# Kernel tuning notes

Measured on AMD Instinct MI355X. Metric: run time of the kernel, lower is better.

Reference implementation:

```python
import jax, jax.numpy as jnp
import numpy as np

N_HEADS, EMB_DIM, K_DIM, V_DIM = 16, 1024, 64, 64
B, L = 4, 2048


def setup_inputs() -> dict:
    key = jax.random.key(0)
    ks = jax.random.split(key, 7)
    scale = 1.0 / np.sqrt(EMB_DIM)
    return {
        "query": jax.random.normal(ks[0], (B, L, EMB_DIM), dtype=jnp.float32),
        "key": jax.random.normal(ks[1], (B, L, EMB_DIM), dtype=jnp.float32),
        "value": jax.random.normal(ks[2], (B, L, EMB_DIM), dtype=jnp.float32),
        "pad_mask": jnp.ones((B, L), dtype=jnp.int32),
        # Linear weights stored as (in, out); torch Linear computes x @ W.T with W (out, in)
        "Wq": jax.random.normal(ks[3], (EMB_DIM, N_HEADS * K_DIM), dtype=jnp.float32) * scale,
        "Wk": jax.random.normal(ks[4], (EMB_DIM, N_HEADS * K_DIM), dtype=jnp.float32) * scale,
        "Wv": jax.random.normal(ks[5], (EMB_DIM, N_HEADS * V_DIM), dtype=jnp.float32) * scale,
        "Wo": jax.random.normal(ks[6], (N_HEADS * V_DIM, EMB_DIM), dtype=jnp.float32) * scale,
    }


def reference(query, key, value, pad_mask, Wq, Wk, Wv, Wo):
    batch, Lq, _ = query.shape
    Lk = key.shape[1]
    # projections -> [B, L, H, dk/dv]
    q = (query @ Wq).reshape(batch, Lq, N_HEADS, K_DIM)
    k = (key @ Wk).reshape(batch, Lk, N_HEADS, K_DIM)
    v = (value @ Wv).reshape(batch, Lk, N_HEADS, V_DIM)
    # logits: [B, H, Lq, Lk], scaled by 1/sqrt(dk)
    logits = jnp.einsum("bqhd,bkhd->bhqk", q, k) / np.sqrt(K_DIM).astype(np.float32)
    # causal mask: disallow j > i
    causal = jnp.tril(jnp.ones((Lq, Lk), dtype=bool))
    logits = jnp.where(causal[None, None], logits, -jnp.inf)
    # pad mask: positions with pad_mask == 0 are masked out
    keep = (pad_mask != 0)[:, None, None, :]  # [B,1,1,Lk]
    logits = jnp.where(keep, logits, -jnp.inf)
    probs = jax.nn.softmax(logits, axis=-1)
    attn = jnp.einsum("bhqk,bkhd->bqhd", probs, v).reshape(batch, Lq, N_HEADS * V_DIM)
    return attn @ Wo
```

## Files before the change

### kernel.cpp

```cpp
#include <hip/hip_runtime.h>
#include <hip/hip_bf16.h>

typedef short bf16x8 __attribute__((ext_vector_type(8)));
typedef float f32x4 __attribute__((ext_vector_type(4)));

#define EMB 1024
#define NH 16
#define SEQ 2048
#define BATCH 4
#define MROWS (BATCH * SEQ)

static __device__ inline unsigned short f2bf(float f) {
  unsigned u = __float_as_uint(f);
  u += 0x7fffu + ((u >> 16) & 1u);
  return (unsigned short)(u >> 16);
}

static __device__ inline unsigned cvtpk(float lo, float hi) {
  unsigned r;
  asm("v_cvt_pk_bf16_f32 %0, %1, %2" : "=v"(r) : "v"(lo), "v"(hi));
  return r;
}

static __device__ inline void gload16(const void* g, void* l) {
  __builtin_amdgcn_global_load_lds(
      (const __attribute__((address_space(1))) unsigned int*)g,
      (__attribute__((address_space(3))) unsigned int*)l, 16, 0, 0);
}

__global__ __launch_bounds__(256) void wtrans_kernel(
    const float* w0, const float* w1, const float* w2, const float* w3,
    unsigned short* o0, unsigned short* o1, unsigned short* o2, unsigned short* o3) {
  __shared__ float t[32][33];
  int z = blockIdx.z;
  const float* W = z == 0 ? w0 : z == 1 ? w1 : z == 2 ? w2 : w3;
  unsigned short* O = z == 0 ? o0 : z == 1 ? o1 : z == 2 ? o2 : o3;
  float sc = (z == 0) ? 0.18033688011112042f : 1.0f;
  int bx = blockIdx.x * 32;
  int by = blockIdx.y * 32;
  int tx = threadIdx.x, ty = threadIdx.y;
#pragma unroll
  for (int j = 0; j < 4; ++j)
    t[ty + j * 8][tx] = W[(size_t)(bx + ty + j * 8) * EMB + by + tx];
  __syncthreads();
#pragma unroll
  for (int j = 0; j < 4; ++j)
    O[(size_t)(by + ty + j * 8) * EMB + bx + tx] = f2bf(t[tx][ty + j * 8] * sc);
}

template <int IN_F32, int OUT_MODE>
__global__ __launch_bounds__(256) void gemm_kernel(const void* Ap, const unsigned short* Bt, void* Cp) {
  __shared__ __align__(16) unsigned short As[128 * 64];
  __shared__ __align__(16) unsigned short Bs[128 * 64];
  const int K = EMB;
  int tid = threadIdx.x;
  int lane = tid & 63, wave = tid >> 6;
  int q = lane & 15, g = lane >> 4;
  int qx7 = q & 7;
  int wm = (wave >> 1) * 64, wn = (wave & 1) * 64;
  int lin = blockIdx.x + (blockIdx.y << 3);
  int idx = (lin & 7) * 64 + (lin >> 3);
  int tm = (idx >> 3) * 128, tn = (idx & 7) * 128;
  f32x4 acc[4][4] = {};
  for (int kt = 0; kt < K; kt += 64) {
    if (IN_F32) {
      const float* A = (const float*)Ap;
#pragma unroll
      for (int it = 0; it < 4; ++it) {
        int gid = tid + it * 256;
        int row = gid >> 3, cb = gid & 7;
        const float4* s0 = (const float4*)(A + (size_t)(tm + row) * K + kt + cb * 8);
        float4 x = s0[0], y = s0[1];
        uint4 w;
        w.x = cvtpk(x.x, x.y); w.y = cvtpk(x.z, x.w);
        w.z = cvtpk(y.x, y.y); w.w = cvtpk(y.z, y.w);
        *(uint4*)&As[row * 64 + 8 * (cb ^ (row & 7))] = w;
      }
    } else {
      const unsigned short* A = (const unsigned short*)Ap;
#pragma unroll
      for (int it = 0; it < 4; ++it) {
        int gid = tid + it * 256;
        int row = gid >> 3, cb = gid & 7;
        gload16(A + (size_t)(tm + row) * K + kt + 8 * (cb ^ (row & 7)), &As[gid * 8]);
      }
    }
#pragma unroll
    for (int it = 0; it < 4; ++it) {
      int gid = tid + it * 256;
      int row = gid >> 3, cb = gid & 7;
      gload16(Bt + (size_t)(tn + row) * K + kt + 8 * (cb ^ (row & 7)), &Bs[gid * 8]);
    }
    __syncthreads();
#pragma unroll
    for (int s = 0; s < 2; ++s) {
      bf16x8 af[4], bfr[4];
#pragma unroll
      for (int mf = 0; mf < 4; ++mf)
        af[mf] = *(const bf16x8*)&As[(wm + mf * 16 + q) * 64 + 8 * ((4 * s + g) ^ qx7)];
#pragma unroll
      for (int nf = 0; nf < 4; ++nf)
        bfr[nf] = *(const bf16x8*)&Bs[(wn + nf * 16 + q) * 64 + 8 * ((4 * s + g) ^ qx7)];
#pragma unroll
      for (int mf = 0; mf < 4; ++mf)
#pragma unroll
        for (int nf = 0; nf < 4; ++nf)
          acc[mf][nf] = __builtin_amdgcn_mfma_f32_16x16x32_bf16(af[mf], bfr[nf], acc[mf][nf], 0, 0, 0);
    }
    __syncthreads();
  }
  if (OUT_MODE == 0) {
    unsigned short* C = (unsigned short*)Cp;
#pragma unroll
    for (int mf = 0; mf < 4; ++mf)
#pragma unroll
      for (int nf = 0; nf < 4; ++nf)
#pragma unroll
        for (int r = 0; r < 4; ++r) {
          int row = tm + wm + mf * 16 + 4 * g + r;
          int col = tn + wn + nf * 16 + q;
          C[(size_t)row * EMB + col] = f2bf(acc[mf][nf][r]);
        }
  } else if (OUT_MODE == 1) {
    unsigned short* C = (unsigned short*)Cp;
#pragma unroll
    for (int mf = 0; mf < 4; ++mf) {
      int m0 = tm + wm + mf * 16 + 4 * g;
      int b = m0 >> 11, l = m0 & 2047;
#pragma unroll
      for (int nf = 0; nf < 4; ++nf) {
        int n = tn + wn + nf * 16 + q;
        int h = n >> 6, dv = n & 63;
        uint2 w;
        w.x = cvtpk(acc[mf][nf][0], acc[mf][nf][1]);
        w.y = cvtpk(acc[mf][nf][2], acc[mf][nf][3]);
        *(uint2*)&C[(((size_t)b * NH + h) * 64 + dv) * SEQ + l] = w;
      }
    }
  } else {
    float* C = (float*)Cp;
#pragma unroll
    for (int mf = 0; mf < 4; ++mf)
#pragma unroll
      for (int nf = 0; nf < 4; ++nf)
#pragma unroll
        for (int r = 0; r < 4; ++r) {
          int row = tm + wm + mf * 16 + 4 * g + r;
          int col = tn + wn + nf * 16 + q;
          C[(size_t)row * EMB + col] = acc[mf][nf][r];
        }
  }
}

__global__ __launch_bounds__(256) void attn_kernel(
    const unsigned short* Qb, const unsigned short* Kb, const unsigned short* VTb,
    const int* pad, unsigned short* Ob) {
  __shared__ __align__(16) unsigned short Ks[2][64 * 64];
  __shared__ __align__(16) unsigned short Vs[2][64 * 64];
  __shared__ __align__(16) unsigned short Ps[4][16 * 64];
  int tid = threadIdx.x;
  int lane = tid & 63, wave = tid >> 6;
  int q = lane & 15, g = lane >> 4;
  int qx7 = q & 7;
  int lin = blockIdx.x;
  int idx = (lin & 7) * 128 + (lin >> 3);
  int b = idx >> 8, h = (idx >> 4) & 15, px = idx & 15;

  int srow = tid >> 3, scb = tid & 7;
  int ssw = 8 * (scb ^ (srow & 7));
  const unsigned short* Kbase = Kb + (size_t)b * SEQ * EMB + (size_t)srow * EMB + h * 64 + ssw;
  const unsigned short* Vbase = VTb + (((size_t)(b * NH + h)) * 64 + srow) * SEQ + ssw;

#pragma unroll 1
  for (int half = 0; half < 2; ++half) {
    int c = half ? 31 - px : px;
    int qg = c * 64 + wave * 16 + q;
    const unsigned short* Qrow = Qb + ((size_t)(b * SEQ + qg)) * EMB + h * 64;
    bf16x8 qf0 = *(const bf16x8*)(Qrow + 8 * g);
    bf16x8 qf1 = *(const bf16x8*)(Qrow + 32 + 8 * g);
    f32x4 o[4] = {};
    float m_run = -INFINITY, l_run = 0.f;

#pragma unroll
    for (int it = 0; it < 2; ++it) {
      gload16(Kbase + (size_t)(it * 32) * EMB, &Ks[0][(tid + it * 256) * 8]);
      gload16(Vbase + it * 32 * SEQ, &Vs[0][(tid + it * 256) * 8]);
    }
    __syncthreads();

#pragma unroll 1
    for (int t = 0; t <= c; ++t) {
      int kvt = t * 64;
      int cur = t & 1;
      if (t < c) {
#pragma unroll
        for (int it = 0; it < 2; ++it) {
          gload16(Kbase + (size_t)(kvt + 64 + it * 32) * EMB, &Ks[cur ^ 1][(tid + it * 256) * 8]);
          gload16(Vbase + (size_t)(kvt + 64) + it * 32 * SEQ, &Vs[cur ^ 1][(tid + it * 256) * 8]);
        }
      }
      int pv = pad[b * SEQ + kvt + lane];
      unsigned long long pmask = __ballot(pv != 0);
      f32x4 sf[4] = {};
      __builtin_amdgcn_s_setprio(1);
#pragma unroll
      for (int s = 0; s < 2; ++s) {
#pragma unroll
        for (int mf = 0; mf < 4; ++mf) {
          bf16x8 kf = *(const bf16x8*)&Ks[cur][(mf * 16 + q) * 64 + 8 * ((4 * s + g) ^ qx7)];
          sf[mf] = __builtin_amdgcn_mfma_f32_16x16x32_bf16(kf, s ? qf1 : qf0, sf[mf], 0, 0, 0);
        }
      }
      __builtin_amdgcn_s_setprio(0);
      float tmax = -INFINITY;
      bool full = (t < c) && (pmask == ~0ull);
      if (full) {
#pragma unroll
        for (int mf = 0; mf < 4; ++mf)
#pragma unroll
          for (int r = 0; r < 4; ++r) tmax = fmaxf(tmax, sf[mf][r]);
      } else {
#pragma unroll
        for (int mf = 0; mf < 4; ++mf)
#pragma unroll
          for (int r = 0; r < 4; ++r) {
            int kvl = mf * 16 + 4 * g + r;
            bool keep = (kvt + kvl <= qg) && ((pmask >> kvl) & 1ULL);
            float sv = keep ? sf[mf][r] : -INFINITY;
            sf[mf][r] = sv;
            tmax = fmaxf(tmax, sv);
          }
      }
      tmax = fmaxf(tmax, __shfl_xor(tmax, 16));
      tmax = fmaxf(tmax, __shfl_xor(tmax, 32));
      if (!__all(tmax <= m_run + 8.0f)) {
        float m_new = fmaxf(m_run, tmax);
        float alpha = __builtin_amdgcn_exp2f(m_run - m_new);
        l_run *= alpha;
#pragma unroll
        for (int mv = 0; mv < 4; ++mv) o[mv] *= alpha;
        m_run = m_new;
      }
      float rsum = 0.f;
      float pvv[16];
#pragma unroll
      for (int mf = 0; mf < 4; ++mf)
#pragma unroll
        for (int r = 0; r < 4; ++r) {
          float p = __builtin_amdgcn_exp2f(sf[mf][r] - m_run);
          pvv[mf * 4 + r] = p;
          rsum += p;
        }
#pragma unroll
      for (int mf = 0; mf < 4; ++mf) {
        uint2 w;
        w.x = cvtpk(pvv[mf * 4 + 0], pvv[mf * 4 + 1]);
        w.y = cvtpk(pvv[mf * 4 + 2], pvv[mf * 4 + 3]);
        int cbP = 2 * mf + (g >> 1);
        *(uint2*)&Ps[wave][q * 64 + 8 * (cbP ^ qx7) + 4 * (g & 1)] = w;
      }
      rsum += __shfl_xor(rsum, 16);
      rsum += __shfl_xor(rsum, 32);
      l_run += rsum;
      __builtin_amdgcn_s_setprio(1);
#pragma unroll
      for (int s = 0; s < 2; ++s) {
        bf16x8 pb = *(const bf16x8*)&Ps[wave][q * 64 + 8 * ((4 * s + g) ^ qx7)];
#pragma unroll
        for (int mv = 0; mv < 4; ++mv) {
          bf16x8 va = *(const bf16x8*)&Vs[cur][(mv * 16 + q) * 64 + 8 * ((4 * s + g) ^ qx7)];
          o[mv] = __builtin_amdgcn_mfma_f32_16x16x32_bf16(va, pb, o[mv], 0, 0, 0);
        }
      }
      __builtin_amdgcn_s_setprio(0);
      __syncthreads();
    }
    float inv = 1.0f / l_run;
    unsigned short* Orow = Ob + ((size_t)(b * SEQ + qg)) * EMB + h * 64;
#pragma unroll
    for (int mv = 0; mv < 4; ++mv) {
      uint2 w;
      w.x = cvtpk(o[mv][0] * inv, o[mv][1] * inv);
      w.y = cvtpk(o[mv][2] * inv, o[mv][3] * inv);
      *(uint2*)&Orow[mv * 16 + 4 * g] = w;
    }
  }
}

extern "C" void kernel_launch(void* const* d_in, const int* in_sizes, int n_in,
                              void* d_out, int out_size, void* d_ws, size_t ws_size,
                              hipStream_t stream) {
  const float* query = (const float*)d_in[0];
  const float* key   = (const float*)d_in[1];
  const float* value = (const float*)d_in[2];
  const int*   pad   = (const int*)d_in[3];
  const float* Wq = (const float*)d_in[4];
  const float* Wk = (const float*)d_in[5];
  const float* Wv = (const float*)d_in[6];
  const float* Wo = (const float*)d_in[7];

  unsigned short* WqT = (unsigned short*)d_ws;
  unsigned short* WkT = WqT + (size_t)EMB * EMB;
  unsigned short* WvT = WkT + (size_t)EMB * EMB;
  unsigned short* WoT = WvT + (size_t)EMB * EMB;
  unsigned short* Qb  = WoT + (size_t)EMB * EMB;
  unsigned short* Kb  = Qb + (size_t)MROWS * EMB;
  unsigned short* VTb = Kb + (size_t)MROWS * EMB;
  unsigned short* Ab  = VTb + (size_t)MROWS * EMB;

  wtrans_kernel<<<dim3(EMB / 32, EMB / 32, 4), dim3(32, 8), 0, stream>>>(
      Wq, Wk, Wv, Wo, WqT, WkT, WvT, WoT);
  gemm_kernel<1, 0><<<dim3(8, 64), 256, 0, stream>>>(query, WqT, Qb);
  gemm_kernel<1, 0><<<dim3(8, 64), 256, 0, stream>>>(key, WkT, Kb);
  gemm_kernel<1, 1><<<dim3(8, 64), 256, 0, stream>>>(value, WvT, VTb);
  attn_kernel<<<dim3(1024), 256, 0, stream>>>(Qb, Kb, VTb, pad, Ab);
  gemm_kernel<0, 2><<<dim3(8, 64), 256, 0, stream>>>(Ab, WoT, d_out);
}
```

Before: 208.4 us.

## Batch QKV projections into one launch and streamline attention softmax inner loop

Merges the three Q/K/V projection GEMMs into a single grid-z launch so 1536 blocks fill the GPU at once instead of three sequential 512-block launches. In attention, the per-tile pad-mask ballots are precomputed into shared memory, and both Q row fragments are loaded up front. The running max is folded into the MFMA accumulator seed so the per-element subtract before exp2 goes away. The setprio hints are removed and masking is applied only on diagonal or padded tiles. This adds register pressure from the extra Q fragments, and changing several things at once makes the effect of each hard to separate.

New measurement: 219.8 us. 5.5% more time.

```diff
diff --git a/kernel.cpp b/kernel.cpp
--- a/kernel.cpp
+++ b/kernel.cpp
@@ -48,8 +48,97 @@
     O[(size_t)(by + ty + j * 8) * EMB + bx + tx] = f2bf(t[tx][ty + j * 8] * sc);
 }
 
-template <int IN_F32, int OUT_MODE>
-__global__ __launch_bounds__(256) void gemm_kernel(const void* Ap, const unsigned short* Bt, void* Cp) {
+__global__ __launch_bounds__(256) void qkv_gemm(
+    const float* qry, const float* key, const float* val,
+    const unsigned short* WqT, const unsigned short* WkT, const unsigned short* WvT,
+    unsigned short* Qb, unsigned short* Kb, unsigned short* VTb) {
+  __shared__ __align__(16) unsigned short As[128 * 64];
+  __shared__ __align__(16) unsigned short Bs[128 * 64];
+  const int K = EMB;
+  int z = blockIdx.z;
+  const float* A = z == 0 ? qry : z == 1 ? key : val;
+  const unsigned short* Bt = z == 0 ? WqT : z == 1 ? WkT : WvT;
+  int tid = threadIdx.x;
+  int lane = tid & 63, wave = tid >> 6;
+  int q = lane & 15, g = lane >> 4;
+  int qx7 = q & 7;
+  int wm = (wave >> 1) * 64, wn = (wave & 1) * 64;
+  int lin = blockIdx.x + (blockIdx.y << 3);
+  int idx = (lin & 7) * 64 + (lin >> 3);
+  int tm = (idx >> 3) * 128, tn = (idx & 7) * 128;
+  f32x4 acc[4][4] = {};
+  for (int kt = 0; kt < K; kt += 64) {
+#pragma unroll
+    for (int it = 0; it < 4; ++it) {
+      int gid = tid + it * 256;
+      int row = gid >> 3, cb = gid & 7;
+      const float4* s0 = (const float4*)(A + (size_t)(tm + row) * K + kt + cb * 8);
+      float4 x = s0[0], y = s0[1];
+      uint4 w;
+      w.x = cvtpk(x.x, x.y); w.y = cvtpk(x.z, x.w);
+      w.z = cvtpk(y.x, y.y); w.w = cvtpk(y.z, y.w);
+      *(uint4*)&As[row * 64 + 8 * (cb ^ (row & 7))] = w;
+    }
+#pragma unroll
+    for (int it = 0; it < 4; ++it) {
+      int gid = tid + it * 256;
+      int row = gid >> 3, cb = gid & 7;
+      gload16(Bt + (size_t)(tn + row) * K + kt + 8 * (cb ^ (row & 7)), &Bs[gid * 8]);
+    }
+    __syncthreads();
+#pragma unroll
+    for (int s = 0; s < 2; ++s) {
+      bf16x8 af[4], bfr[4];
+#pragma unroll
+      for (int mf = 0; mf < 4; ++mf)
+        af[mf] = *(const bf16x8*)&As[(wm + mf * 16 + q) * 64 + 8 * ((4 * s + g) ^ qx7)];
+#pragma unroll
+      for (int nf = 0; nf < 4; ++nf)
+        bfr[nf] = *(const bf16x8*)&Bs[(wn + nf * 16 + q) * 64 + 8 * ((4 * s + g) ^ qx7)];
+#pragma unroll
+      for (int mf = 0; mf < 4; ++mf)
+#pragma unroll
+        for (int nf = 0; nf < 4; ++nf)
+          acc[mf][nf] = __builtin_amdgcn_mfma_f32_16x16x32_bf16(af[mf], bfr[nf], acc[mf][nf], 0, 0, 0);
+    }
+    __syncthreads();
+  }
+  if (z != 2) {
+    unsigned short* C = z == 0 ? Qb : Kb;
+#pragma unroll
+    for (int mf = 0; mf < 4; ++mf)
+#pragma unroll
+      for (int nf = 0; nf < 4; ++nf) {
+        int row = tm + wm + mf * 16 + 4 * g;
+        int col = tn + wn + nf * 16 + q;
+        uint2 w;
+        w.x = cvtpk(acc[mf][nf][0], acc[mf][nf][1]);
+        w.y = cvtpk(acc[mf][nf][2], acc[mf][nf][3]);
+        C[(size_t)(row + 0) * EMB + col] = (unsigned short)(w.x & 0xffff);
+        C[(size_t)(row + 1) * EMB + col] = (unsigned short)(w.x >> 16);
+        C[(size_t)(row + 2) * EMB + col] = (unsigned short)(w.y & 0xffff);
+        C[(size_t)(row + 3) * EMB + col] = (unsigned short)(w.y >> 16);
+      }
+  } else {
+    unsigned short* C = VTb;
+#pragma unroll
+    for (int mf = 0; mf < 4; ++mf) {
+      int m0 = tm + wm + mf * 16 + 4 * g;
+      int b = m0 >> 11, l = m0 & 2047;
+#pragma unroll
+      for (int nf = 0; nf < 4; ++nf) {
+        int n = tn + wn + nf * 16 + q;
+        int h = n >> 6, dv = n & 63;
+        uint2 w;
+        w.x = cvtpk(acc[mf][nf][0], acc[mf][nf][1]);
+        w.y = cvtpk(acc[mf][nf][2], acc[mf][nf][3]);
+        *(uint2*)&C[(((size_t)b * NH + h) * 64 + dv) * SEQ + l] = w;
+      }
+    }
+  }
+}
+
+__global__ __launch_bounds__(256) void out_gemm(const unsigned short* Ab, const unsigned short* Bt, float* Cp) {
   __shared__ __align__(16) unsigned short As[128 * 64];
   __shared__ __align__(16) unsigned short Bs[128 * 64];
   const int K = EMB;
@@ -63,32 +152,11 @@
   int tm = (idx >> 3) * 128, tn = (idx & 7) * 128;
   f32x4 acc[4][4] = {};
   for (int kt = 0; kt < K; kt += 64) {
-    if (IN_F32) {
-      const float* A = (const float*)Ap;
-#pragma unroll
-      for (int it = 0; it < 4; ++it) {
-        int gid = tid + it * 256;
-        int row = gid >> 3, cb = gid & 7;
-        const float4* s0 = (const float4*)(A + (size_t)(tm + row) * K + kt + cb * 8);
-        float4 x = s0[0], y = s0[1];
-        uint4 w;
-        w.x = cvtpk(x.x, x.y); w.y = cvtpk(x.z, x.w);
-        w.z = cvtpk(y.x, y.y); w.w = cvtpk(y.z, y.w);
-        *(uint4*)&As[row * 64 + 8 * (cb ^ (row & 7))] = w;
-      }
-    } else {
-      const unsigned short* A = (const unsigned short*)Ap;
-#pragma unroll
-      for (int it = 0; it < 4; ++it) {
-        int gid = tid + it * 256;
-        int row = gid >> 3, cb = gid & 7;
-        gload16(A + (size_t)(tm + row) * K + kt + 8 * (cb ^ (row & 7)), &As[gid * 8]);
-      }
-    }
 #pragma unroll
     for (int it = 0; it < 4; ++it) {
       int gid = tid + it * 256;
       int row = gid >> 3, cb = gid & 7;
+      gload16(Ab + (size_t)(tm + row) * K + kt + 8 * (cb ^ (row & 7)), &As[gid * 8]);
       gload16(Bt + (size_t)(tn + row) * K + kt + 8 * (cb ^ (row & 7)), &Bs[gid * 8]);
     }
     __syncthreads();
@@ -109,47 +177,16 @@
     }
     __syncthreads();
   }
-  if (OUT_MODE == 0) {
-    unsigned short* C = (unsigned short*)Cp;
-#pragma unroll
-    for (int mf = 0; mf < 4; ++mf)
-#pragma unroll
-      for (int nf = 0; nf < 4; ++nf)
-#pragma unroll
-        for (int r = 0; r < 4; ++r) {
-          int row = tm + wm + mf * 16 + 4 * g + r;
-          int col = tn + wn + nf * 16 + q;
-          C[(size_t)row * EMB + col] = f2bf(acc[mf][nf][r]);
-        }
-  } else if (OUT_MODE == 1) {
-    unsigned short* C = (unsigned short*)Cp;
-#pragma unroll
-    for (int mf = 0; mf < 4; ++mf) {
-      int m0 = tm + wm + mf * 16 + 4 * g;
-      int b = m0 >> 11, l = m0 & 2047;
-#pragma unroll
-      for (int nf = 0; nf < 4; ++nf) {
-        int n = tn + wn + nf * 16 + q;
-        int h = n >> 6, dv = n & 63;
-        uint2 w;
-        w.x = cvtpk(acc[mf][nf][0], acc[mf][nf][1]);
-        w.y = cvtpk(acc[mf][nf][2], acc[mf][nf][3]);
-        *(uint2*)&C[(((size_t)b * NH + h) * 64 + dv) * SEQ + l] = w;
-      }
-    }
-  } else {
-    float* C = (float*)Cp;
-#pragma unroll
-    for (int mf = 0; mf < 4; ++mf)
-#pragma unroll
-      for (int nf = 0; nf < 4; ++nf)
-#pragma unroll
-        for (int r = 0; r < 4; ++r) {
-          int row = tm + wm + mf * 16 + 4 * g + r;
-          int col = tn + wn + nf * 16 + q;
-          C[(size_t)row * EMB + col] = acc[mf][nf][r];
-        }
-  }
+#pragma unroll
+  for (int mf = 0; mf < 4; ++mf)
+#pragma unroll
+    for (int nf = 0; nf < 4; ++nf)
+#pragma unroll
+      for (int r = 0; r < 4; ++r) {
+        int row = tm + wm + mf * 16 + 4 * g + r;
+        int col = tn + wn + nf * 16 + q;
+        Cp[(size_t)row * EMB + col] = acc[mf][nf][r];
+      }
 }
 
 __global__ __launch_bounds__(256) void attn_kernel(
@@ -158,6 +195,7 @@
   __shared__ __align__(16) unsigned short Ks[2][64 * 64];
   __shared__ __align__(16) unsigned short Vs[2][64 * 64];
   __shared__ __align__(16) unsigned short Ps[4][16 * 64];
+  __shared__ unsigned long long pm[32];
   int tid = threadIdx.x;
   int lane = tid & 63, wave = tid >> 6;
   int q = lane & 15, g = lane >> 4;
@@ -165,6 +203,25 @@
   int lin = blockIdx.x;
   int idx = (lin & 7) * 128 + (lin >> 3);
   int b = idx >> 8, h = (idx >> 4) & 15, px = idx & 15;
+  int cA = px, cB = 31 - px;
+
+#pragma unroll
+  for (int i = 0; i < 8; ++i) {
+    int t = wave * 8 + i;
+    int pv = pad[b * SEQ + t * 64 + lane];
+    unsigned long long msk = __ballot(pv != 0);
+    if (lane == 0) pm[t] = msk;
+  }
+
+  int qgA = cA * 64 + wave * 16 + q;
+  int qgB = cB * 64 + wave * 16 + q;
+  const unsigned short* QrowA = Qb + ((size_t)(b * SEQ + qgA)) * EMB + h * 64;
+  const unsigned short* QrowB = Qb + ((size_t)(b * SEQ + qgB)) * EMB + h * 64;
+  bf16x8 qfh[2][2];
+  qfh[0][0] = *(const bf16x8*)(QrowA + 8 * g);
+  qfh[0][1] = *(const bf16x8*)(QrowA + 32 + 8 * g);
+  qfh[1][0] = *(const bf16x8*)(QrowB + 8 * g);
+  qfh[1][1] = *(const bf16x8*)(QrowB + 32 + 8 * g);
 
   int srow = tid >> 3, scb = tid & 7;
   int ssw = 8 * (scb ^ (srow & 7));
@@ -173,18 +230,16 @@
 
 #pragma unroll 1
   for (int half = 0; half < 2; ++half) {
-    int c = half ? 31 - px : px;
-    int qg = c * 64 + wave * 16 + q;
-    const unsigned short* Qrow = Qb + ((size_t)(b * SEQ + qg)) * EMB + h * 64;
-    bf16x8 qf0 = *(const bf16x8*)(Qrow + 8 * g);
-    bf16x8 qf1 = *(const bf16x8*)(Qrow + 32 + 8 * g);
+    int c = half ? cB : cA;
+    int qg = half ? qgB : qgA;
+    bf16x8 qf0 = qfh[half][0], qf1 = qfh[half][1];
     f32x4 o[4] = {};
-    float m_run = -INFINITY, l_run = 0.f;
+    float m_run = 0.f, l_run = 0.f;
 
 #pragma unroll
     for (int it = 0; it < 2; ++it) {
       gload16(Kbase + (size_t)(it * 32) * EMB, &Ks[0][(tid + it * 256) * 8]);
-      gload16(Vbase + it * 32 * SEQ, &Vs[0][(tid + it * 256) * 8]);
+      gload16(Vbase + (size_t)(it * 32) * SEQ, &Vs[0][(tid + it * 256) * 8]);
     }
     __syncthreads();
 
@@ -196,13 +251,16 @@
 #pragma unroll
         for (int it = 0; it < 2; ++it) {
           gload16(Kbase + (size_t)(kvt + 64 + it * 32) * EMB, &Ks[cur ^ 1][(tid + it * 256) * 8]);
-          gload16(Vbase + (size_t)(kvt + 64) + it * 32 * SEQ, &Vs[cur ^ 1][(tid + it * 256) * 8]);
+          gload16(Vbase + (size_t)(kvt + 64) + (size_t)(it * 32) * SEQ, &Vs[cur ^ 1][(tid + it * 256) * 8]);
         }
       }
-      int pv = pad[b * SEQ + kvt + lane];
-      unsigned long long pmask = __ballot(pv != 0);
-      f32x4 sf[4] = {};
-      __builtin_amdgcn_s_setprio(1);
+      unsigned long long pmask = pm[t];
+      bool notfull = (pmask != ~0ull);
+
+      f32x4 sf[4];
+      f32x4 seed = {-m_run, -m_run, -m_run, -m_run};
+#pragma unroll
+      for (int mf = 0; mf < 4; ++mf) sf[mf] = seed;
 #pragma unroll
       for (int s = 0; s < 2; ++s) {
 #pragma unroll
@@ -211,43 +269,46 @@
           sf[mf] = __builtin_amdgcn_mfma_f32_16x16x32_bf16(kf, s ? qf1 : qf0, sf[mf], 0, 0, 0);
         }
       }
-      __builtin_amdgcn_s_setprio(0);
-      float tmax = -INFINITY;
-      bool full = (t < c) && (pmask == ~0ull);
-      if (full) {
-#pragma unroll
-        for (int mf = 0; mf < 4; ++mf)
-#pragma unroll
-          for (int r = 0; r < 4; ++r) tmax = fmaxf(tmax, sf[mf][r]);
-      } else {
+
+      if (t == c || notfull) {
 #pragma unroll
         for (int mf = 0; mf < 4; ++mf)
 #pragma unroll
           for (int r = 0; r < 4; ++r) {
             int kvl = mf * 16 + 4 * g + r;
             bool keep = (kvt + kvl <= qg) && ((pmask >> kvl) & 1ULL);
-            float sv = keep ? sf[mf][r] : -INFINITY;
-            sf[mf][r] = sv;
-            tmax = fmaxf(tmax, sv);
+            sf[mf][r] = keep ? sf[mf][r] : -INFINITY;
           }
       }
+
+      float t0 = fmaxf(fmaxf(sf[0][0], sf[0][1]), fmaxf(sf[0][2], sf[0][3]));
+      float t1 = fmaxf(fmaxf(sf[1][0], sf[1][1]), fmaxf(sf[1][2], sf[1][3]));
+      float t2 = fmaxf(fmaxf(sf[2][0], sf[2][1]), fmaxf(sf[2][2], sf[2][3]));
+      float t3 = fmaxf(fmaxf(sf[3][0], sf[3][1]), fmaxf(sf[3][2], sf[3][3]));
+      float tmax = fmaxf(fmaxf(t0, t1), fmaxf(t2, t3));
       tmax = fmaxf(tmax, __shfl_xor(tmax, 16));
       tmax = fmaxf(tmax, __shfl_xor(tmax, 32));
-      if (!__all(tmax <= m_run + 8.0f)) {
-        float m_new = fmaxf(m_run, tmax);
-        float alpha = __builtin_amdgcn_exp2f(m_run - m_new);
+
+      if (!__all(tmax <= 8.0f)) {
+        float d = fmaxf(tmax, 0.f);
+        float alpha = __builtin_amdgcn_exp2f(-d);
         l_run *= alpha;
 #pragma unroll
         for (int mv = 0; mv < 4; ++mv) o[mv] *= alpha;
-        m_run = m_new;
-      }
+#pragma unroll
+        for (int mf = 0; mf < 4; ++mf)
+#pragma unroll
+          for (int r = 0; r < 4; ++r) sf[mf][r] -= d;
+        m_run += d;
+      }
+
       float rsum = 0.f;
       float pvv[16];
 #pragma unroll
       for (int mf = 0; mf < 4; ++mf)
 #pragma unroll
         for (int r = 0; r < 4; ++r) {
-          float p = __builtin_amdgcn_exp2f(sf[mf][r] - m_run);
+          float p = __builtin_amdgcn_exp2f(sf[mf][r]);
           pvv[mf * 4 + r] = p;
           rsum += p;
         }
@@ -262,7 +323,7 @@
       rsum += __shfl_xor(rsum, 16);
       rsum += __shfl_xor(rsum, 32);
       l_run += rsum;
-      __builtin_amdgcn_s_setprio(1);
+
 #pragma unroll
       for (int s = 0; s < 2; ++s) {
         bf16x8 pb = *(const bf16x8*)&Ps[wave][q * 64 + 8 * ((4 * s + g) ^ qx7)];
@@ -272,9 +333,9 @@
           o[mv] = __builtin_amdgcn_mfma_f32_16x16x32_bf16(va, pb, o[mv], 0, 0, 0);
         }
       }
-      __builtin_amdgcn_s_setprio(0);
       __syncthreads();
     }
+
     float inv = 1.0f / l_run;
     unsigned short* Orow = Ob + ((size_t)(b * SEQ + qg)) * EMB + h * 64;
 #pragma unroll
@@ -310,9 +371,7 @@
 
   wtrans_kernel<<<dim3(EMB / 32, EMB / 32, 4), dim3(32, 8), 0, stream>>>(
       Wq, Wk, Wv, Wo, WqT, WkT, WvT, WoT);
-  gemm_kernel<1, 0><<<dim3(8, 64), 256, 0, stream>>>(query, WqT, Qb);
-  gemm_kernel<1, 0><<<dim3(8, 64), 256, 0, stream>>>(key, WkT, Kb);
-  gemm_kernel<1, 1><<<dim3(8, 64), 256, 0, stream>>>(value, WvT, VTb);
+  qkv_gemm<<<dim3(8, 64, 3), 256, 0, stream>>>(query, key, value, WqT, WkT, WvT, Qb, Kb, VTb);
   attn_kernel<<<dim3(1024), 256, 0, stream>>>(Qb, Kb, VTb, pad, Ab);
-  gemm_kernel<0, 2><<<dim3(8, 64), 256, 0, stream>>>(Ab, WoT, d_out);
-}
+  out_gemm<<<dim3(8, 64), 256, 0, stream>>>(Ab, WoT, (float*)d_out);
+}
```
